# Optimization experiments

Hardware: AMD Instinct MI355X
Metric: run time of the kernel (lower is better)

The kernel has to match this reference:

```python
import jax, jax.numpy as jnp
import numpy as np
import math

B, L, DIM = 2, 2048, 2048
N_HEADS, N_KV = 16, 4
HD = DIM // N_HEADS          # 128
N_REP = N_HEADS // N_KV      # 4
THETA = 10000.0


def setup_inputs() -> dict:
    key = jax.random.key(0)
    ks = jax.random.split(key, 6)
    x = jax.random.normal(ks[0], (B, L, DIM), dtype=jnp.float32)
    # rotary phasor freqs_cis = exp(i * t * inv_freq), stored as cos/sin
    inv_freq = 1.0 / (THETA ** (jnp.arange(0, HD, 2, dtype=jnp.float32) / HD))  # [HD//2]
    ang = jnp.arange(L, dtype=jnp.float32)[:, None] * inv_freq[None, :]          # [L, HD//2]
    freqs_cos = jnp.cos(ang)
    freqs_sin = jnp.sin(ang)
    s = 0.02
    wq = jax.random.normal(ks[1], (DIM, DIM), dtype=jnp.float32) * s
    wk = jax.random.normal(ks[2], (N_KV * HD, DIM), dtype=jnp.float32) * s
    wv = jax.random.normal(ks[3], (N_KV * HD, DIM), dtype=jnp.float32) * s
    wo = jax.random.normal(ks[4], (DIM, DIM), dtype=jnp.float32) * s
    return {"x": x, "freqs_cos": freqs_cos, "freqs_sin": freqs_sin,
            "wq": wq, "wk": wk, "wv": wv, "wo": wo}


def _apply_rope(t, cos, sin):
    # t: [B, L, H, HD]; cos/sin: [L, HD//2] -> broadcast [1, L, 1, HD//2]
    tr = t.reshape(*t.shape[:-1], HD // 2, 2)
    t0, t1 = tr[..., 0], tr[..., 1]
    c = cos[None, :, None, :]
    s = sin[None, :, None, :]
    r0 = t0 * c - t1 * s
    r1 = t0 * s + t1 * c
    return jnp.stack([r0, r1], axis=-1).reshape(t.shape)


def reference(x, freqs_cos, freqs_sin, wq, wk, wv, wo):
    Bx, Lx, _ = x.shape
    xq = (x @ wq.T).reshape(Bx, Lx, N_HEADS, HD)
    xk = (x @ wk.T).reshape(Bx, Lx, N_KV, HD)
    xv = (x @ wv.T).reshape(Bx, Lx, N_KV, HD)
    xq = _apply_rope(xq, freqs_cos, freqs_sin)
    xk = _apply_rope(xk, freqs_cos, freqs_sin)
    # repeat_kv (GQA expansion) then [B, H, L, HD]
    keys = jnp.repeat(xk, N_REP, axis=2).transpose(0, 2, 1, 3)
    values = jnp.repeat(xv, N_REP, axis=2).transpose(0, 2, 1, 3)
    q = xq.transpose(0, 2, 1, 3)
    scores = jnp.einsum('bhqd,bhkd->bhqk', q, keys) / math.sqrt(HD)
    mask = jnp.triu(jnp.full((Lx, Lx), -jnp.inf, dtype=scores.dtype), k=1)
    scores = scores + mask[None, None]
    probs = jax.nn.softmax(scores.astype(jnp.float32), axis=-1).astype(q.dtype)
    out = jnp.einsum('bhqk,bhkd->bhqd', probs, values)
    out = out.transpose(0, 2, 1, 3).reshape(Bx, Lx, -1)
    output = out @ wo.T
    return (output, keys, values)
```

## Files before the change

### kernel.cpp

```cpp
#include <hip/hip_runtime.h>
#include <hip/hip_bf16.h>

using bf16x8 = __attribute__((ext_vector_type(8))) short;
using f32x4  = __attribute__((ext_vector_type(4))) float;

__device__ __forceinline__ unsigned short f32_to_bf16(float f) {
  unsigned u = __float_as_uint(f);
  u += 0x7FFFu + ((u >> 16) & 1u);
  return (unsigned short)(u >> 16);
}
__device__ __forceinline__ unsigned pack2(float lo, float hi) {
  __hip_bfloat162 h = __float22bfloat162_rn(make_float2(lo, hi));
  return *reinterpret_cast<unsigned*>(&h);
}
__device__ __forceinline__ void gload_lds16(const void* g, void* l) {
  __builtin_amdgcn_global_load_lds(
      (const __attribute__((address_space(1))) unsigned int*)g,
      (__attribute__((address_space(3))) unsigned int*)l, 16, 0, 0);
}

__global__ void cast_all_kernel(const float* __restrict__ wq, const float* __restrict__ wo,
                                const float* __restrict__ wk, const float* __restrict__ wv,
                                const float* __restrict__ x,
                                unsigned short* __restrict__ WQKV,
                                unsigned short* __restrict__ WO,
                                unsigned short* __restrict__ XBF) {
  int i = blockIdx.x * blockDim.x + threadIdx.x;
  const float4* s; ushort4* d; int j;
  if (i < 1048576)      { s = (const float4*)wq; d = (ushort4*)WQKV;            j = i; }
  else if (i < 2097152) { s = (const float4*)wo; d = (ushort4*)WO;              j = i - 1048576; }
  else if (i < 2359296) { s = (const float4*)wk; d = (ushort4*)WQKV + 1048576;  j = i - 2097152; }
  else if (i < 2621440) { s = (const float4*)wv; d = (ushort4*)WQKV + 1310720;  j = i - 2359296; }
  else                  { s = (const float4*)x;  d = (ushort4*)XBF;             j = i - 2621440; }
  float4 v = s[j];
  ushort4 o;
  o.x = f32_to_bf16(v.x); o.y = f32_to_bf16(v.y);
  o.z = f32_to_bf16(v.z); o.w = f32_to_bf16(v.w);
  d[j] = o;
}

template <int BM, int MODE>
__global__ __launch_bounds__(512, 2) void gemm256_kernel(
    const unsigned short* __restrict__ A, const unsigned short* __restrict__ Bw,
    float* __restrict__ C, unsigned short* __restrict__ qbf_out,
    float* __restrict__ xkv_out, int M, int N, int K) {
  constexpr int ABYTES = BM * 128;
  constexpr int BBYTES = 256 * 128;
  constexpr int BUFB   = ABYTES + BBYTES;
  constexpr int ALOADS = BM / 64;
  constexpr int WROWS  = BM / 32;
  __shared__ __align__(16) char Lsh[2 * BUFB];

  const int tid = threadIdx.x;
  const int wid = tid >> 6, lane = tid & 63;
  const int lr = lane & 15, lg = lane >> 4;
  const int wr = wid >> 2, wc = wid & 3;
  const int bn = blockIdx.x, bm = blockIdx.y;
  const int x0 = lg * 16;

  f32x4 acc[WROWS][4] = {};

  const char* Ag = (const char*)A + (size_t)(bm * BM) * K * 2;
  const char* Bg = (const char*)Bw + (size_t)(bn * 256) * K * 2;

  int aoff[ALOADS], boff[4];
#pragma unroll
  for (int i = 0; i < ALOADS; ++i) {
    int lin = wid * (BM * 16) + i * 1024 + lane * 16;
    int grow = lin >> 7;
    int gcol = (lin & 127) ^ ((grow & 7) << 4);
    aoff[i] = grow * (K * 2) + gcol;
  }
#pragma unroll
  for (int i = 0; i < 4; ++i) {
    int lin = wid * 4096 + i * 1024 + lane * 16;
    int grow = lin >> 7;
    int gcol = (lin & 127) ^ ((grow & 7) << 4);
    boff[i] = grow * (K * 2) + gcol;
  }

  auto stage = [&](int s, int buf) {
    const int kb = s * 128;
    char* Lb = Lsh + buf * BUFB;
#pragma unroll
    for (int i = 0; i < ALOADS; ++i)
      gload_lds16(Ag + aoff[i] + kb, Lb + wid * (BM * 16) + i * 1024);
#pragma unroll
    for (int i = 0; i < 4; ++i)
      gload_lds16(Bg + boff[i] + kb, Lb + ABYTES + wid * 4096 + i * 1024);
  };

  auto kstep = [&](char* Lb) {
    bf16x8 bfr[4][2];
#pragma unroll
    for (int fc = 0; fc < 4; ++fc) {
      const int row = wc * 64 + fc * 16 + lr;
      const int base = ABYTES + row * 128;
      const int sw = (row & 7) << 4;
#pragma unroll
      for (int ks = 0; ks < 2; ++ks)
        bfr[fc][ks] = *reinterpret_cast<const bf16x8*>(Lb + base + ((ks * 64 + x0) ^ sw));
    }
#pragma unroll
    for (int q = 0; q < WROWS / 2; ++q) {
      bf16x8 af[2][2];
#pragma unroll
      for (int t = 0; t < 2; ++t) {
        const int row = wr * (BM / 2) + (2 * q + t) * 16 + lr;
        const int base = row * 128;
        const int sw = (row & 7) << 4;
#pragma unroll
        for (int ks = 0; ks < 2; ++ks)
          af[t][ks] = *reinterpret_cast<const bf16x8*>(Lb + base + ((ks * 64 + x0) ^ sw));
      }
      asm volatile("s_waitcnt lgkmcnt(0)" ::: "memory");
      __builtin_amdgcn_sched_barrier(0);
      __builtin_amdgcn_s_setprio(1);
#pragma unroll
      for (int t = 0; t < 2; ++t)
#pragma unroll
        for (int fc = 0; fc < 4; ++fc) {
          acc[2 * q + t][fc] = __builtin_amdgcn_mfma_f32_16x16x32_bf16(af[t][0], bfr[fc][0], acc[2 * q + t][fc], 0, 0, 0);
          acc[2 * q + t][fc] = __builtin_amdgcn_mfma_f32_16x16x32_bf16(af[t][1], bfr[fc][1], acc[2 * q + t][fc], 0, 0, 0);
        }
      __builtin_amdgcn_s_setprio(0);
    }
  };

  const int NST = K >> 6;
  stage(0, 0);
  for (int it = 0; it < NST / 2; ++it) {
    __builtin_amdgcn_s_barrier();
    stage(2 * it + 1, 1);
    if constexpr (BM == 256) asm volatile("s_waitcnt vmcnt(8)" ::: "memory");
    else                     asm volatile("s_waitcnt vmcnt(6)" ::: "memory");
    __builtin_amdgcn_s_barrier();
    kstep(Lsh);
    __builtin_amdgcn_s_barrier();
    if (it < NST / 2 - 1) {
      stage(2 * it + 2, 0);
      if constexpr (BM == 256) asm volatile("s_waitcnt vmcnt(8)" ::: "memory");
      else                     asm volatile("s_waitcnt vmcnt(6)" ::: "memory");
    } else {
      asm volatile("s_waitcnt vmcnt(0)" ::: "memory");
    }
    __builtin_amdgcn_s_barrier();
    kstep(Lsh + BUFB);
  }

  if constexpr (MODE == 0) {
#pragma unroll
    for (int fr = 0; fr < WROWS; ++fr) {
      const int m = bm * BM + wr * (BM / 2) + fr * 16 + lg * 4;
#pragma unroll
      for (int fc = 0; fc < 4; ++fc) {
        const int n = bn * 256 + wc * 64 + fc * 16 + lr;
#pragma unroll
        for (int r = 0; r < 4; ++r)
          C[(size_t)(m + r) * N + n] = acc[fr][fc][r];
      }
    }
  } else {
    if (bn < 8) {
#pragma unroll
      for (int fr = 0; fr < WROWS; ++fr) {
        const int m = bm * BM + wr * (BM / 2) + fr * 16 + lg * 4;
#pragma unroll
        for (int fc = 0; fc < 4; ++fc) {
          const int n = bn * 256 + wc * 64 + fc * 16 + lr;
#pragma unroll
          for (int r = 0; r < 4; ++r)
            qbf_out[(size_t)(m + r) * 2048 + n] = f32_to_bf16(acc[fr][fc][r]);
        }
      }
    } else {
#pragma unroll
      for (int fr = 0; fr < WROWS; ++fr) {
        const int m = bm * BM + wr * (BM / 2) + fr * 16 + lg * 4;
#pragma unroll
        for (int fc = 0; fc < 4; ++fc) {
          const int n = bn * 256 + wc * 64 + fc * 16 + lr - 2048;
#pragma unroll
          for (int r = 0; r < 4; ++r)
            xkv_out[(size_t)(m + r) * 1024 + n] = acc[fr][fc][r];
        }
      }
    }
  }
}

__global__ void kv_proc_kernel(const float* __restrict__ xkv, const float* __restrict__ fc,
                               const float* __restrict__ fs, unsigned short* __restrict__ kbf,
                               float* __restrict__ keys, unsigned short* __restrict__ vt,
                               float* __restrict__ values) {
  int bid = blockIdx.x;
  if (bid < 4096) {
    int idx = bid * 256 + threadIdx.x;
    int i = idx & 63;
    int kvh = (idx >> 6) & 3;
    int l = (idx >> 8) & 2047;
    int b = idx >> 19;
    float2 t = reinterpret_cast<const float2*>(xkv)[(size_t)(b * 2048 + l) * 512 + kvh * 64 + i];
    float c = fc[l * 64 + i], s = fs[l * 64 + i];
    float r0 = t.x * c - t.y * s;
    float r1 = t.x * s + t.y * c;
    int kidx = ((b * 4 + kvh) * 2048 + l) * 64 + i;
    ushort2 o; o.x = f32_to_bf16(r0); o.y = f32_to_bf16(r1);
    reinterpret_cast<ushort2*>(kbf)[kidx] = o;
    float2 f; f.x = r0; f.y = r1;
#pragma unroll
    for (int rep = 0; rep < 4; ++rep) {
      int h = kvh * 4 + rep;
      reinterpret_cast<float2*>(keys)[((b * 16 + h) * 2048 + l) * 64 + i] = f;
    }
  } else {
    int idx = (bid - 4096) * 256 + threadIdx.x;
    int d = idx & 127;
    int kvh = (idx >> 7) & 3;
    int l = (idx >> 9) & 2047;
    int b = idx >> 20;
    float v = xkv[(size_t)(b * 2048 + l) * 1024 + 512 + kvh * 128 + d];
#pragma unroll
    for (int rep = 0; rep < 4; ++rep) {
      int h = kvh * 4 + rep;
      values[((size_t)(b * 16 + h) * 2048 + l) * 128 + d] = v;
    }
    vt[((size_t)(b * 4 + kvh) * 128 + d) * 2048 + l] = f32_to_bf16(v);
  }
}

__global__ __launch_bounds__(256) void attn_kernel(
    const unsigned short* __restrict__ qbf, const float* __restrict__ fc,
    const float* __restrict__ fs, const unsigned short* __restrict__ kbf,
    const unsigned short* __restrict__ vt, unsigned short* __restrict__ obf) {
  __shared__ unsigned short Ks[64 * 128];
  __shared__ unsigned short Vs[128 * 64];
  const int tid = threadIdx.x;
  const int w = tid >> 6, lane = tid & 63;
  const int lr = lane & 15, lg = lane >> 4;
  const int bid = blockIdx.x;
  const int qt = 15 - (bid >> 5);
  const int bh = bid & 31;
  const int b = bh >> 4, h = bh & 15, kv = h >> 2;
  const int q0 = qt * 128 + w * 32;
  const float ALPHA = 0.08838834764831845f;
  const int swz = (lr & 7) << 4;

  bf16x8 qf[2][4];
#pragma unroll
  for (int t = 0; t < 2; ++t) {
    const int qrow = q0 + t * 16 + lr;
    const unsigned short* xqp = qbf + (size_t)(b * 2048 + qrow) * 2048 + h * 128;
    const float* fcp = fc + qrow * 64;
    const float* fsp = fs + qrow * 64;
#pragma unroll
    for (int s = 0; s < 4; ++s) {
      union { bf16x8 v8; unsigned short us[8]; } rw;
      rw.v8 = *reinterpret_cast<const bf16x8*>(xqp + s * 32 + lg * 8);
      float xv[8];
#pragma unroll
      for (int k = 0; k < 8; ++k) xv[k] = __uint_as_float(((unsigned)rw.us[k]) << 16);
      float4 c4 = *reinterpret_cast<const float4*>(fcp + s * 16 + lg * 4);
      float4 s4 = *reinterpret_cast<const float4*>(fsp + s * 16 + lg * 4);
      c4.x *= ALPHA; c4.y *= ALPHA; c4.z *= ALPHA; c4.w *= ALPHA;
      s4.x *= ALPHA; s4.y *= ALPHA; s4.z *= ALPHA; s4.w *= ALPHA;
      union { bf16x8 v8; unsigned u[4]; } uu;
      uu.u[0] = pack2(xv[0] * c4.x - xv[1] * s4.x, xv[0] * s4.x + xv[1] * c4.x);
      uu.u[1] = pack2(xv[2] * c4.y - xv[3] * s4.y, xv[2] * s4.y + xv[3] * c4.y);
      uu.u[2] = pack2(xv[4] * c4.z - xv[5] * s4.z, xv[4] * s4.z + xv[5] * c4.z);
      uu.u[3] = pack2(xv[6] * c4.w - xv[7] * s4.w, xv[6] * s4.w + xv[7] * c4.w);
      qf[t][s] = uu.v8;
    }
  }

  f32x4 acc[2][8] = {};
  float mrow[2] = {-1e30f, -1e30f}, lsum[2] = {0.f, 0.f};

  const char* kgbase = (const char*)(kbf + (size_t)(b * 4 + kv) * 2048 * 128);
  const char* vgbase = (const char*)(vt + (size_t)(b * 4 + kv) * 128 * 2048);

  int ksrc[4], vsrc[4];
#pragma unroll
  for (int i = 0; i < 4; ++i) {
    int p = w * 4096 + i * 1024 + lane * 16;
    int krow = p >> 8;
    int kperm = ((krow >> 5) << 5) + ((krow >> 4) & 1) + (((krow >> 2) & 3) << 3) + ((krow & 3) << 1);
    int kcol = (p & 255) ^ ((krow & 7) << 4);
    ksrc[i] = kperm * 256 + kcol;
    int drow = p >> 7;
    int dcol = (p & 127) ^ ((drow & 7) << 4);
    vsrc[i] = drow * 4096 + dcol;
  }

  const int nblocks = 2 * qt + 2;
  for (int j = 0; j < nblocks; ++j) {
    const int kb = j * 64;
    __syncthreads();
#pragma unroll
    for (int i = 0; i < 4; ++i) {
      gload_lds16(kgbase + (size_t)kb * 256 + ksrc[i], (char*)Ks + w * 4096 + i * 1024);
      gload_lds16(vgbase + (size_t)kb * 2 + vsrc[i], (char*)Vs + w * 4096 + i * 1024);
    }
    __syncthreads();
    if (j == nblocks - 1 && w < 2) continue;
    f32x4 sT[2][4];
#pragma unroll
    for (int c = 0; c < 4; ++c) {
      bf16x8 kf[4];
#pragma unroll
      for (int s = 0; s < 4; ++s)
        kf[s] = *reinterpret_cast<const bf16x8*>((char*)Ks + (((c * 16 + lr) * 256 + s * 64 + lg * 16) ^ swz));
      f32x4 t0 = {0.f, 0.f, 0.f, 0.f}, t1 = {0.f, 0.f, 0.f, 0.f};
#pragma unroll
      for (int s = 0; s < 4; ++s) {
        t0 = __builtin_amdgcn_mfma_f32_16x16x32_bf16(kf[s], qf[0][s], t0, 0, 0, 0);
        t1 = __builtin_amdgcn_mfma_f32_16x16x32_bf16(kf[s], qf[1][s], t1, 0, 0, 0);
      }
      sT[0][c] = t0; sT[1][c] = t1;
    }
    bf16x8 ptf[2][2];
#pragma unroll
    for (int t = 0; t < 2; ++t) {
      const int qrow = q0 + t * 16 + lr;
      float x[4][4];
      float mt = -1e30f;
#pragma unroll
      for (int c = 0; c < 4; ++c)
#pragma unroll
        for (int r = 0; r < 4; ++r) {
          int ka = kb + ((c >> 1) << 5) + (c & 1) + 8 * lg + 2 * r;
          float v = (ka <= qrow) ? sT[t][c][r] : -1e30f;
          x[c][r] = v;
          mt = fmaxf(mt, v);
        }
      mt = fmaxf(mt, __shfl_xor(mt, 16));
      mt = fmaxf(mt, __shfl_xor(mt, 32));
      const bool skip = __all(mt <= mrow[t] + 8.0f);
      float mnew, fac;
      if (skip) {
        mnew = mrow[t];
      } else {
        mnew = fmaxf(mrow[t], mt);
        fac = __expf(mrow[t] - mnew);
        mrow[t] = mnew;
      }
      float rs = 0.f;
      float pv[4][4];
#pragma unroll
      for (int c = 0; c < 4; ++c)
#pragma unroll
        for (int r = 0; r < 4; ++r) {
          float p = __expf(x[c][r] - mnew);
          pv[c][r] = p;
          rs += p;
        }
      rs += __shfl_xor(rs, 16);
      rs += __shfl_xor(rs, 32);
      if (skip) {
        lsum[t] += rs;
      } else {
        lsum[t] = lsum[t] * fac + rs;
#pragma unroll
        for (int dt = 0; dt < 8; ++dt)
#pragma unroll
          for (int r = 0; r < 4; ++r) acc[t][dt][r] *= fac;
      }
#pragma unroll
      for (int kk = 0; kk < 2; ++kk) {
        union { bf16x8 v8; unsigned u[4]; } uu;
#pragma unroll
        for (int wd = 0; wd < 4; ++wd)
          uu.u[wd] = pack2(pv[2 * kk][wd], pv[2 * kk + 1][wd]);
        ptf[t][kk] = uu.v8;
      }
    }
#pragma unroll
    for (int dt = 0; dt < 8; ++dt) {
      bf16x8 v0 = *reinterpret_cast<const bf16x8*>((char*)Vs + (((dt * 16 + lr) * 128 + lg * 16) ^ swz));
      bf16x8 v1 = *reinterpret_cast<const bf16x8*>((char*)Vs + (((dt * 16 + lr) * 128 + 64 + lg * 16) ^ swz));
      acc[0][dt] = __builtin_amdgcn_mfma_f32_16x16x32_bf16(v0, ptf[0][0], acc[0][dt], 0, 0, 0);
      acc[0][dt] = __builtin_amdgcn_mfma_f32_16x16x32_bf16(v1, ptf[0][1], acc[0][dt], 0, 0, 0);
      acc[1][dt] = __builtin_amdgcn_mfma_f32_16x16x32_bf16(v0, ptf[1][0], acc[1][dt], 0, 0, 0);
      acc[1][dt] = __builtin_amdgcn_mfma_f32_16x16x32_bf16(v1, ptf[1][1], acc[1][dt], 0, 0, 0);
    }
  }
#pragma unroll
  for (int t = 0; t < 2; ++t) {
    float inv = 1.0f / lsum[t];
#pragma unroll
    for (int dt = 0; dt < 8; ++dt) {
      ushort4 o;
      o.x = f32_to_bf16(acc[t][dt][0] * inv);
      o.y = f32_to_bf16(acc[t][dt][1] * inv);
      o.z = f32_to_bf16(acc[t][dt][2] * inv);
      o.w = f32_to_bf16(acc[t][dt][3] * inv);
      *reinterpret_cast<ushort4*>(obf + ((size_t)(b * 2048 + q0 + t * 16 + lr)) * 2048 + h * 128 + dt * 16 + lg * 4) = o;
    }
  }
}

extern "C" void kernel_launch(void* const* d_in, const int* in_sizes, int n_in,
                              void* d_out, int out_size, void* d_ws, size_t ws_size,
                              hipStream_t stream) {
  const float* x  = (const float*)d_in[0];
  const float* fc = (const float*)d_in[1];
  const float* fs = (const float*)d_in[2];
  const float* wq = (const float*)d_in[3];
  const float* wk = (const float*)d_in[4];
  const float* wv = (const float*)d_in[5];
  const float* wo = (const float*)d_in[6];

  float* out    = (float*)d_out;
  float* keys   = out + 8388608;
  float* values = out + 16777216;

  char* ws = (char*)d_ws;
  unsigned short* WQKV = (unsigned short*)(ws + 0);
  unsigned short* WO   = (unsigned short*)(ws + 12582912);
  unsigned short* XBF  = (unsigned short*)(ws + 20971520);
  unsigned short* QBF  = (unsigned short*)(ws + 37748736);
  float*          XKV  = (float*)(ws + 54525952);
  unsigned short* KBF  = (unsigned short*)(ws + 88080384);
  unsigned short* VTB  = (unsigned short*)(ws + 92274688);
  unsigned short* ATT  = XBF;

  cast_all_kernel<<<18432, 256, 0, stream>>>(wq, wo, wk, wv, x, WQKV, WO, XBF);

  gemm256_kernel<256, 1><<<dim3(12, 16), 512, 0, stream>>>(
      XBF, WQKV, nullptr, QBF, XKV, 4096, 3072, 2048);

  kv_proc_kernel<<<12288, 256, 0, stream>>>(XKV, fc, fs, KBF, keys, VTB, values);

  attn_kernel<<<512, 256, 0, stream>>>(QBF, fc, fs, KBF, VTB, ATT);

  gemm256_kernel<128, 0><<<dim3(8, 32), 512, 0, stream>>>(
      ATT, WO, out, nullptr, nullptr, 4096, 2048, 2048);
}
```

Before: 222.7 us.

## Overlap Wo bf16 cast with QKV GEMM and vectorize KV processing

Moves the fp32-to-bf16 conversion of the output-projection weight out of the up-front cast kernel and into extra idle blocks of the QKV GEMM grid (grid widened from 12 to 16 columns). This lets the cast run alongside GEMM tiles on CUs the 192-block GEMM would otherwise leave idle, and it shortens the serial cast kernel. The KV RoPE/expansion kernel is also changed to process four floats per thread with float4 loads and stores, which cuts its block count. The vt transpose writes stay scalar and strided, and the extra GEMM blocks compete with the GEMM for bandwidth.

```diff
diff --git a/kernel.cpp b/kernel.cpp
--- a/kernel.cpp
+++ b/kernel.cpp
@@ -19,19 +19,16 @@
       (__attribute__((address_space(3))) unsigned int*)l, 16, 0, 0);
 }
 
-__global__ void cast_all_kernel(const float* __restrict__ wq, const float* __restrict__ wo,
-                                const float* __restrict__ wk, const float* __restrict__ wv,
-                                const float* __restrict__ x,
+__global__ void cast_all_kernel(const float* __restrict__ wq, const float* __restrict__ wk,
+                                const float* __restrict__ wv, const float* __restrict__ x,
                                 unsigned short* __restrict__ WQKV,
-                                unsigned short* __restrict__ WO,
                                 unsigned short* __restrict__ XBF) {
   int i = blockIdx.x * blockDim.x + threadIdx.x;
   const float4* s; ushort4* d; int j;
   if (i < 1048576)      { s = (const float4*)wq; d = (ushort4*)WQKV;            j = i; }
-  else if (i < 2097152) { s = (const float4*)wo; d = (ushort4*)WO;              j = i - 1048576; }
-  else if (i < 2359296) { s = (const float4*)wk; d = (ushort4*)WQKV + 1048576;  j = i - 2097152; }
-  else if (i < 2621440) { s = (const float4*)wv; d = (ushort4*)WQKV + 1310720;  j = i - 2359296; }
-  else                  { s = (const float4*)x;  d = (ushort4*)XBF;             j = i - 2621440; }
+  else if (i < 1310720) { s = (const float4*)wk; d = (ushort4*)WQKV + 1048576;  j = i - 1048576; }
+  else if (i < 1572864) { s = (const float4*)wv; d = (ushort4*)WQKV + 1310720;  j = i - 1310720; }
+  else                  { s = (const float4*)x;  d = (ushort4*)XBF;             j = i - 1572864; }
   float4 v = s[j];
   ushort4 o;
   o.x = f32_to_bf16(v.x); o.y = f32_to_bf16(v.y);
@@ -43,7 +40,8 @@
 __global__ __launch_bounds__(512, 2) void gemm256_kernel(
     const unsigned short* __restrict__ A, const unsigned short* __restrict__ Bw,
     float* __restrict__ C, unsigned short* __restrict__ qbf_out,
-    float* __restrict__ xkv_out, int M, int N, int K) {
+    float* __restrict__ xkv_out, const float* __restrict__ wo_src,
+    unsigned short* __restrict__ wo_dst, int M, int N, int K) {
   constexpr int ABYTES = BM * 128;
   constexpr int BBYTES = 256 * 128;
   constexpr int BUFB   = ABYTES + BBYTES;
@@ -51,11 +49,26 @@
   constexpr int WROWS  = BM / 32;
   __shared__ __align__(16) char Lsh[2 * BUFB];
 
+  const int bn = blockIdx.x, bm = blockIdx.y;
+  if constexpr (MODE == 1) {
+    if (bn >= 12) {
+      int base = ((bn - 12) * 16 + bm) * 512 + threadIdx.x;
+#pragma unroll 4
+      for (int i = base; i < 1048576; i += 32768) {
+        float4 v = reinterpret_cast<const float4*>(wo_src)[i];
+        ushort4 o;
+        o.x = f32_to_bf16(v.x); o.y = f32_to_bf16(v.y);
+        o.z = f32_to_bf16(v.z); o.w = f32_to_bf16(v.w);
+        reinterpret_cast<ushort4*>(wo_dst)[i] = o;
+      }
+      return;
+    }
+  }
+
   const int tid = threadIdx.x;
   const int wid = tid >> 6, lane = tid & 63;
   const int lr = lane & 15, lg = lane >> 4;
   const int wr = wid >> 2, wc = wid & 3;
-  const int bn = blockIdx.x, bm = blockIdx.y;
   const int x0 = lg * 16;
 
   f32x4 acc[WROWS][4] = {};
@@ -194,38 +207,45 @@
                                float* __restrict__ keys, unsigned short* __restrict__ vt,
                                float* __restrict__ values) {
   int bid = blockIdx.x;
-  if (bid < 4096) {
+  if (bid < 2048) {
     int idx = bid * 256 + threadIdx.x;
-    int i = idx & 63;
-    int kvh = (idx >> 6) & 3;
-    int l = (idx >> 8) & 2047;
-    int b = idx >> 19;
-    float2 t = reinterpret_cast<const float2*>(xkv)[(size_t)(b * 2048 + l) * 512 + kvh * 64 + i];
-    float c = fc[l * 64 + i], s = fs[l * 64 + i];
-    float r0 = t.x * c - t.y * s;
-    float r1 = t.x * s + t.y * c;
-    int kidx = ((b * 4 + kvh) * 2048 + l) * 64 + i;
-    ushort2 o; o.x = f32_to_bf16(r0); o.y = f32_to_bf16(r1);
-    reinterpret_cast<ushort2*>(kbf)[kidx] = o;
-    float2 f; f.x = r0; f.y = r1;
+    int i2 = idx & 31;
+    int kvh = (idx >> 5) & 3;
+    int l = (idx >> 7) & 2047;
+    int b = idx >> 18;
+    float4 t = reinterpret_cast<const float4*>(xkv)[(size_t)(b * 2048 + l) * 256 + kvh * 32 + i2];
+    float2 c2 = reinterpret_cast<const float2*>(fc)[l * 32 + i2];
+    float2 s2 = reinterpret_cast<const float2*>(fs)[l * 32 + i2];
+    float4 r;
+    r.x = t.x * c2.x - t.y * s2.x;
+    r.y = t.x * s2.x + t.y * c2.x;
+    r.z = t.z * c2.y - t.w * s2.y;
+    r.w = t.z * s2.y + t.w * c2.y;
+    ushort4 o;
+    o.x = f32_to_bf16(r.x); o.y = f32_to_bf16(r.y);
+    o.z = f32_to_bf16(r.z); o.w = f32_to_bf16(r.w);
+    reinterpret_cast<ushort4*>(kbf)[((b * 4 + kvh) * 2048 + l) * 32 + i2] = o;
 #pragma unroll
     for (int rep = 0; rep < 4; ++rep) {
       int h = kvh * 4 + rep;
-      reinterpret_cast<float2*>(keys)[((b * 16 + h) * 2048 + l) * 64 + i] = f;
+      reinterpret_cast<float4*>(keys)[((size_t)(b * 16 + h) * 2048 + l) * 32 + i2] = r;
     }
   } else {
-    int idx = (bid - 4096) * 256 + threadIdx.x;
-    int d = idx & 127;
-    int kvh = (idx >> 7) & 3;
-    int l = (idx >> 9) & 2047;
-    int b = idx >> 20;
-    float v = xkv[(size_t)(b * 2048 + l) * 1024 + 512 + kvh * 128 + d];
+    int idx = (bid - 2048) * 256 + threadIdx.x;
+    int dq = idx & 31;
+    int kvh = (idx >> 5) & 3;
+    int l = (idx >> 7) & 2047;
+    int b = idx >> 18;
+    float4 v = reinterpret_cast<const float4*>(xkv)[(size_t)(b * 2048 + l) * 256 + 128 + kvh * 32 + dq];
 #pragma unroll
     for (int rep = 0; rep < 4; ++rep) {
       int h = kvh * 4 + rep;
-      values[((size_t)(b * 16 + h) * 2048 + l) * 128 + d] = v;
-    }
-    vt[((size_t)(b * 4 + kvh) * 128 + d) * 2048 + l] = f32_to_bf16(v);
+      reinterpret_cast<float4*>(values)[((size_t)(b * 16 + h) * 2048 + l) * 32 + dq] = v;
+    }
+    vt[((size_t)(b * 4 + kvh) * 128 + 4 * dq + 0) * 2048 + l] = f32_to_bf16(v.x);
+    vt[((size_t)(b * 4 + kvh) * 128 + 4 * dq + 1) * 2048 + l] = f32_to_bf16(v.y);
+    vt[((size_t)(b * 4 + kvh) * 128 + 4 * dq + 2) * 2048 + l] = f32_to_bf16(v.z);
+    vt[((size_t)(b * 4 + kvh) * 128 + 4 * dq + 3) * 2048 + l] = f32_to_bf16(v.w);
   }
 }
 
@@ -424,15 +444,15 @@
   unsigned short* VTB  = (unsigned short*)(ws + 92274688);
   unsigned short* ATT  = XBF;
 
-  cast_all_kernel<<<18432, 256, 0, stream>>>(wq, wo, wk, wv, x, WQKV, WO, XBF);
-
-  gemm256_kernel<256, 1><<<dim3(12, 16), 512, 0, stream>>>(
-      XBF, WQKV, nullptr, QBF, XKV, 4096, 3072, 2048);
-
-  kv_proc_kernel<<<12288, 256, 0, stream>>>(XKV, fc, fs, KBF, keys, VTB, values);
+  cast_all_kernel<<<14336, 256, 0, stream>>>(wq, wk, wv, x, WQKV, XBF);
+
+  gemm256_kernel<256, 1><<<dim3(16, 16), 512, 0, stream>>>(
+      XBF, WQKV, nullptr, QBF, XKV, wo, WO, 4096, 3072, 2048);
+
+  kv_proc_kernel<<<4096, 256, 0, stream>>>(XKV, fc, fs, KBF, keys, VTB, values);
 
   attn_kernel<<<512, 256, 0, stream>>>(QBF, fc, fs, KBF, VTB, ATT);
 
   gemm256_kernel<128, 0><<<dim3(8, 32), 512, 0, stream>>>(
-      ATT, WO, out, nullptr, nullptr, 4096, 2048, 2048);
-}
+      ATT, WO, out, nullptr, nullptr, nullptr, nullptr, 4096, 2048, 2048);
+}
```

Result: no change. 226.1 us (+1.5%).
